# Optimization experiments

Measured on AMD Instinct MI355X. Metric: run time of the kernel, lower is better.

## Reference

```python
import jax, jax.numpy as jnp
import numpy as np
from jax import lax

N, C, H, W = 6, 64, 128, 128
BN_EPS = 1e-5


def setup_inputs() -> dict:
    key = jax.random.key(0)
    ks = jax.random.split(key, 16)
    def p(i, shape, scale=0.05):
        return jax.random.normal(ks[i], shape, jnp.float32) * scale
    return {
        "raw_feat": jax.random.normal(ks[0], (N, C, H, W), jnp.float32),
        # PixelWeightedFusionSoftmax params (1x1 convs stored as [out,in] matrices)
        "pw_w1": p(1, (4, C)), "pw_b1": p(2, (4,)),
        "bn_gamma": 1.0 + p(3, (4,)), "bn_beta": p(4, (4,)),
        "bn_mean": jnp.zeros((4,), jnp.float32), "bn_var": jnp.ones((4,), jnp.float32),
        "pw_w2": p(5, (1, 4)), "pw_b2": p(6, (1,)),
        # ConvMod params: a = dwconv11x11(gelu(conv1x1_{2C->C}(q))); out = proj(a * v(v) * att_map)
        "cm_a1_w": p(7, (C, 2 * C)), "cm_a1_b": p(8, (C,)),
        "cm_dw_w": p(9, (C, 1, 11, 11)), "cm_dw_b": p(10, (C,)),
        "cm_v_w": p(11, (C, C)), "cm_v_b": p(12, (C,)),
        "cm_proj_w": p(13, (C, C)), "cm_proj_b": p(14, (C,)),
    }


def _conf_maps(x, pw_w1, pw_b1, bn_gamma, bn_beta, bn_mean, bn_var, pw_w2, pw_b2):
    # x: [N,C,H,W] -> per-agent confidence maps [N,1,H,W], min-max normalized per agent
    h = jnp.einsum('nchw,oc->nohw', x, pw_w1) + pw_b1[:, None, None]
    scale = (bn_gamma / jnp.sqrt(bn_var + BN_EPS))[:, None, None]
    h = (h - bn_mean[:, None, None]) * scale + bn_beta[:, None, None]  # BN eval mode
    h = jax.nn.relu(h)
    h = jax.nn.relu(jnp.einsum('nchw,oc->nohw', h, pw_w2) + pw_b2[:, None, None])
    mn = h.min(axis=(1, 2, 3), keepdims=True)
    mx = h.max(axis=(1, 2, 3), keepdims=True)
    return (h - mn) / (mx - mn)


def reference(raw_feat, pw_w1, pw_b1, bn_gamma, bn_beta, bn_mean, bn_var, pw_w2, pw_b2,
              cm_a1_w, cm_a1_b, cm_dw_w, cm_dw_b, cm_v_w, cm_v_b, cm_proj_w, cm_proj_b):
    conf = _conf_maps(raw_feat, pw_w1, pw_b1, bn_gamma, bn_beta, bn_mean, bn_var, pw_w2, pw_b2)  # [N,1,H,W]
    # att_map[i,k] = (1 - conf_i) * conf_k
    att_map = (1.0 - conf)[:, None] * conf[None, :]  # [N,N,1,H,W]
    # q[i,k] = concat(raw[i], raw[k]) along channels -> [N,N,2C,H,W]
    q = jnp.concatenate([jnp.broadcast_to(raw_feat[:, None], (N, N, C, H, W)),
                         jnp.broadcast_to(raw_feat[None, :], (N, N, C, H, W))], axis=2)
    a = jax.nn.gelu(jnp.einsum('ikchw,oc->ikohw', q, cm_a1_w) + cm_a1_b[:, None, None],
                    approximate=False)
    a = lax.conv_general_dilated(a.reshape(N * N, C, H, W), cm_dw_w,
                                 window_strides=(1, 1), padding='SAME',
                                 feature_group_count=C,
                                 dimension_numbers=('NCHW', 'OIHW', 'NCHW'))
    a = a.reshape(N, N, C, H, W) + cm_dw_b[:, None, None]
    vproj = jnp.einsum('nchw,oc->nohw', raw_feat, cm_v_w) + cm_v_b[:, None, None]  # [N,C,H,W]
    x = a * vproj[None] * att_map  # [N,N,C,H,W]
    out = jnp.einsum('ikchw,oc->ikohw', x, cm_proj_w) + cm_proj_b[:, None, None]
    updated = raw_feat + out.sum(axis=1)  # ego i accumulates over all senders k
    return updated.reshape(N * C, H, W)   # matches torch.cat(local_com_mat_update, dim=0)
```

## Files before the change

### kernel.cpp

```cpp
#include <hip/hip_runtime.h>
#include <math.h>

#define NAG 6
#define CC  64
#define HH  128
#define WW  128
#define HWT 16384
#define HWP 8192
#define BN_EPS 1e-5f
#define WFRAG_PJ_OFF (24 * 64 * 8)

typedef unsigned int u32;
typedef __fp16 f16x2v __attribute__((ext_vector_type(2)));
typedef __fp16 f16x8  __attribute__((ext_vector_type(8)));
typedef float  f32x4  __attribute__((ext_vector_type(4)));

__device__ __forceinline__ float gelu_fast(float x) {
    float s = x * x;
    float m = fmaf(s, -0.10294535f, -2.30226045f);
    float e = __builtin_amdgcn_exp2f(x * m);
    return x * __builtin_amdgcn_rcpf(1.0f + e);
}

__global__ void k_init(u32* __restrict__ mm) {
    int t = threadIdx.x;
    if (t < NAG) mm[t] = 0x7F800000u;
    else if (t < 2 * NAG) mm[t] = 0u;
}

__global__ __launch_bounds__(256) void k_wprep(
    const float* __restrict__ a1w, const float* __restrict__ vw,
    const float* __restrict__ pjw, __fp16* __restrict__ wfrag)
{
    int t = blockIdx.x * 256 + threadIdx.x;
    if (t >= 32 * 64) return;
    int lane = t & 63;
    int slot = t >> 6;
    bool pj = slot >= 24;
    int s = pj ? slot - 24 : slot;
    int ot = s >> 1, kf = s & 1;
    int o  = (pj ? ot : (ot & 3)) * 16 + (lane & 15);
    int ch = kf * 32 + (lane >> 4) * 8;
    const float* src;
    if (pj)          src = pjw + o * CC + ch;
    else if (ot < 4) src = a1w + o * 2 * CC + ch;
    else if (ot < 8) src = a1w + o * 2 * CC + CC + ch;
    else             src = vw  + o * CC + ch;
    __fp16* dst = wfrag + ((size_t)slot * 64 + lane) * 8;
    #pragma unroll
    for (int j = 0; j < 8; ++j) dst[j] = (__fp16)src[j];
}

__global__ __launch_bounds__(256) void k_conf(
    const float* __restrict__ raw,
    const float* __restrict__ w1, const float* __restrict__ b1,
    const float* __restrict__ gamma, const float* __restrict__ beta,
    const float* __restrict__ mean, const float* __restrict__ var,
    const float* __restrict__ w2, const float* __restrict__ b2,
    float* __restrict__ conf, u32* __restrict__ mm)
{
    const int n = blockIdx.y;
    const int p = blockIdx.x * 256 + threadIdx.x;
    const float* x = raw + (size_t)(n * CC) * HWT + p;

    float a[4] = {0.f, 0.f, 0.f, 0.f};
    #pragma unroll 8
    for (int c = 0; c < CC; ++c) {
        float v = x[c * HWT];
        a[0] = fmaf(w1[0 * CC + c], v, a[0]);
        a[1] = fmaf(w1[1 * CC + c], v, a[1]);
        a[2] = fmaf(w1[2 * CC + c], v, a[2]);
        a[3] = fmaf(w1[3 * CC + c], v, a[3]);
    }
    float h2 = b2[0];
    #pragma unroll
    for (int o = 0; o < 4; ++o) {
        float sc = gamma[o] * rsqrtf(var[o] + BN_EPS);
        float hb = (a[o] + b1[o] - mean[o]) * sc + beta[o];
        hb = fmaxf(hb, 0.f);
        h2 = fmaf(w2[o], hb, h2);
    }
    h2 = fmaxf(h2, 0.f);
    conf[n * HWT + p] = h2;

    float mn = h2, mx = h2;
    #pragma unroll
    for (int off = 32; off > 0; off >>= 1) {
        mn = fminf(mn, __shfl_xor(mn, off, 64));
        mx = fmaxf(mx, __shfl_xor(mx, off, 64));
    }
    __shared__ float smn[4], smx[4];
    int wid = threadIdx.x >> 6, lane = threadIdx.x & 63;
    if (lane == 0) { smn[wid] = mn; smx[wid] = mx; }
    __syncthreads();
    if (threadIdx.x == 0) {
        mn = fminf(fminf(smn[0], smn[1]), fminf(smn[2], smn[3]));
        mx = fmaxf(fmaxf(smx[0], smx[1]), fmaxf(smx[2], smx[3]));
        atomicMin(&mm[n], __float_as_uint(mn));
        atomicMax(&mm[n + NAG], __float_as_uint(mx));
    }
}

__global__ __launch_bounds__(256) void k_pqv(
    const float* __restrict__ raw, const __fp16* __restrict__ wfrag,
    const float* __restrict__ vb, const float* __restrict__ conf,
    const u32* __restrict__ mm,
    u32* __restrict__ Ph, u32* __restrict__ Qh, u32* __restrict__ Wh)
{
    const int n   = blockIdx.y;
    const int px0 = blockIdx.x * 128;
    const int t = threadIdx.x, lane = t & 63, wv = t >> 6;
    const int lm = lane & 15, kg = lane >> 4;
    const int pxw = px0 + wv * 32;
    const int pxl = pxw + lm;
    const int pxs = pxw + kg * 4;

    const float* rawn = raw + (size_t)n * CC * HWT;

    f16x8 afr[2][2];
    #pragma unroll
    for (int mt = 0; mt < 2; ++mt) {
        #pragma unroll
        for (int kf = 0; kf < 2; ++kf) {
            const float* base = rawn + (size_t)(kf * 32 + kg * 8) * HWT + pxl + mt * 16;
            f16x8 a;
            #pragma unroll
            for (int p = 0; p < 4; ++p) {
                f16x2v h = __builtin_amdgcn_cvt_pkrtz(base[(2 * p) * HWT],
                                                      base[(2 * p + 1) * HWT]);
                a[2 * p] = h.x; a[2 * p + 1] = h.y;
            }
            afr[mt][kf] = a;
        }
    }

    const float mn = __uint_as_float(mm[n]);
    const float mx = __uint_as_float(mm[n + NAG]);
    const float inv = 1.f / (mx - mn);
    f32x4 cn[2];
    #pragma unroll
    for (int mt = 0; mt < 2; ++mt) {
        f32x4 cv = *(const f32x4*)(conf + n * HWT + pxs + mt * 16);
        cn[mt] = (cv - mn) * inv;
    }

    #pragma unroll
    for (int ot = 0; ot < 12; ++ot) {
        f16x8 b0 = *(const f16x8*)(wfrag + ((size_t)(ot * 2 + 0) * 64 + lane) * 8);
        f16x8 b1 = *(const f16x8*)(wfrag + ((size_t)(ot * 2 + 1) * 64 + lane) * 8);
        const int o = (ot & 3) * 16 + lm;
        #pragma unroll
        for (int mt = 0; mt < 2; ++mt) {
            f32x4 acc = (f32x4){0.f, 0.f, 0.f, 0.f};
            acc = __builtin_amdgcn_mfma_f32_16x16x32_f16(afr[mt][0], b0, acc, 0, 0, 0);
            acc = __builtin_amdgcn_mfma_f32_16x16x32_f16(afr[mt][1], b1, acc, 0, 0, 0);
            const int pxb = pxs + mt * 16;
            f32x4 r;
            u32* plane;
            if (ot < 8) {
                r = acc;
                plane = (ot < 4 ? Ph : Qh) + (size_t)(n * CC + o) * HWP + (pxb >> 1);
            } else {
                r = (acc + vb[o]) * cn[mt];
                plane = Wh + (size_t)(n * CC + o) * HWP + (pxb >> 1);
            }
            f16x2v h0 = __builtin_amdgcn_cvt_pkrtz(r[0], r[1]);
            f16x2v h1 = __builtin_amdgcn_cvt_pkrtz(r[2], r[3]);
            *(uint2*)plane = make_uint2(__builtin_bit_cast(u32, h0),
                                        __builtin_bit_cast(u32, h1));
        }
    }
}

#define GPITCH 88
#define GROWS  74
#define GDW    (GROWS * GPITCH / 2)
#define NU2    13

__global__ __launch_bounds__(256, 3) void k_main(
    const u32* __restrict__ Ph, const u32* __restrict__ Qh,
    const u32* __restrict__ Wh, const float* __restrict__ conf,
    const u32* __restrict__ mm,
    const float* __restrict__ a1b, const float* __restrict__ dww,
    const float* __restrict__ dwb, u32* __restrict__ Sh)
{
    const int tile = blockIdx.x;
    const int c    = blockIdx.y;
    const int i    = blockIdx.z;
    const int y0 = (tile >> 1) * 64;
    const int x0 = (tile & 1) * 64;
    const int t    = threadIdx.x;
    const int lane = t & 63;
    const int ty   = t >> 6;
    const int lm   = lane & 15;
    const int kg   = lane >> 4;
    const int kg8  = kg * 8;

    __shared__ __align__(16) u32 GT32[2 * GDW];

    const float bdw = dwb[c];
    const float ba1 = a1b[c];

    const float* wc = dww + c * 121;
    f16x8 afrag[11];
    #pragma unroll
    for (int dy = 0; dy < 11; ++dy) {
        f16x8 a;
        #pragma unroll
        for (int j = 0; j < 8; ++j) {
            int d = kg8 + j - lm - 3;
            int dcl = min(max(d, 0), 10);
            float wv = wc[dy * 11 + dcl];
            a[j] = (__fp16)((d == dcl) ? wv : 0.f);
        }
        afrag[dy] = a;
    }

    f16x2v bias2; bias2.x = (__fp16)ba1; bias2.y = (__fp16)ba1;

    int offs[NU2];
    u32 preg[NU2];
    const u32* Pc = Ph + (size_t)(i * CC + c) * HWP;
    #pragma unroll
    for (int u = 0; u < NU2; ++u) {
        int d = t + u * 256;
        int row = d / (GPITCH / 2);
        int cp  = d - row * (GPITCH / 2);
        int gy = y0 + row - 5;
        int gx = x0 + 2 * cp - 8;
        bool inb = (d < GDW) && (gy >= 0) && (gy < HH) && (gx >= 0) && (gx < WW);
        offs[u] = inb ? (gy * (WW / 2) + (gx >> 1)) : -1;
        u32 p = 0u;
        if (inb) {
            f16x2v ph = __builtin_bit_cast(f16x2v, Pc[offs[u]]) + bias2;
            p = __builtin_bit_cast(u32, ph);
        }
        preg[u] = p;
    }

    const int oy  = y0 + ty * 16 + lm;
    const int obx = x0 + kg * 4;
    const int obase = oy * WW + obx;
    const int rowb = (ty * 16 + lm) * GPITCH + kg8;

    f32x4 sacc[4];
    #pragma unroll
    for (int tx = 0; tx < 4; ++tx) sacc[tx] = (f32x4){0.f, 0.f, 0.f, 0.f};

    u32 qreg[NU2];
    {
        const u32* Qc = Qh + (size_t)(0 * CC + c) * HWP;
        #pragma unroll
        for (int u = 0; u < NU2; ++u)
            qreg[u] = (offs[u] >= 0) ? Qc[offs[u]] : 0u;
    }
    #pragma unroll
    for (int u = 0; u < NU2; ++u) {
        int d = t + u * 256;
        if (u < NU2 - 1 || d < GDW) {
            f16x2v s = __builtin_bit_cast(f16x2v, preg[u]) +
                       __builtin_bit_cast(f16x2v, qreg[u]);
            float g0 = gelu_fast((float)s.x);
            float g1 = gelu_fast((float)s.y);
            GT32[d] = __builtin_bit_cast(u32, __builtin_amdgcn_cvt_pkrtz(g0, g1));
        }
    }
    {
        const u32* Qc = Qh + (size_t)(1 * CC + c) * HWP;
        #pragma unroll
        for (int u = 0; u < NU2; ++u)
            qreg[u] = (offs[u] >= 0) ? Qc[offs[u]] : 0u;
    }
    __syncthreads();

    #pragma unroll 1
    for (int k = 0; k < NAG; ++k) {
        const u32* Wc = Wh + (size_t)(k * CC + c) * HWP + (obase >> 1);
        uint2 wv[4];
        #pragma unroll
        for (int tx = 0; tx < 4; ++tx)
            wv[tx] = *(const uint2*)(Wc + 8 * tx);

        const __fp16* GTh = (const __fp16*)(GT32 + (k & 1) * GDW);
        #pragma unroll
        for (int tx = 0; tx < 4; ++tx) {
            f32x4 acc = (f32x4){0.f, 0.f, 0.f, 0.f};
            #pragma unroll
            for (int dy = 0; dy < 11; ++dy) {
                f16x8 b = *(const f16x8*)(GTh + rowb + dy * GPITCH + 16 * tx);
                acc = __builtin_amdgcn_mfma_f32_16x16x32_f16(afrag[dy], b, acc, 0, 0, 0);
            }
            f16x2v w0 = __builtin_bit_cast(f16x2v, wv[tx].x);
            f16x2v w1 = __builtin_bit_cast(f16x2v, wv[tx].y);
            f32x4 wf = (f32x4){(float)w0.x, (float)w0.y, (float)w1.x, (float)w1.y};
            sacc[tx] += (acc + bdw) * wf;
        }

        if (k + 1 < NAG) {
            u32* GW = GT32 + ((k + 1) & 1) * GDW;
            #pragma unroll
            for (int u = 0; u < NU2; ++u) {
                int d = t + u * 256;
                if (u < NU2 - 1 || d < GDW) {
                    f16x2v s = __builtin_bit_cast(f16x2v, preg[u]) +
                               __builtin_bit_cast(f16x2v, qreg[u]);
                    float g0 = gelu_fast((float)s.x);
                    float g1 = gelu_fast((float)s.y);
                    GW[d] = __builtin_bit_cast(u32, __builtin_amdgcn_cvt_pkrtz(g0, g1));
                }
            }
            if (k + 2 < NAG) {
                const u32* Qc = Qh + (size_t)((k + 2) * CC + c) * HWP;
                #pragma unroll
                for (int u = 0; u < NU2; ++u)
                    qreg[u] = (offs[u] >= 0) ? Qc[offs[u]] : 0u;
            }
            __syncthreads();
        }
    }

    const float mn = __uint_as_float(mm[i]);
    const float mx = __uint_as_float(mm[i + NAG]);
    const float inv = 1.f / (mx - mn);
    const float* cfi = conf + i * HWT + obase;
    u32* Sc = Sh + (size_t)(i * CC + c) * HWP + (obase >> 1);
    #pragma unroll
    for (int tx = 0; tx < 4; ++tx) {
        f32x4 cv = *(const f32x4*)(cfi + 16 * tx);
        f32x4 r = sacc[tx] * (1.f - (cv - mn) * inv);
        f16x2v h0 = __builtin_amdgcn_cvt_pkrtz(r[0], r[1]);
        f16x2v h1 = __builtin_amdgcn_cvt_pkrtz(r[2], r[3]);
        *(uint2*)(Sc + 8 * tx) = make_uint2(__builtin_bit_cast(u32, h0),
                                            __builtin_bit_cast(u32, h1));
    }
}

__global__ __launch_bounds__(256) void k_out(
    const u32* __restrict__ Sh, const float* __restrict__ raw,
    const __fp16* __restrict__ wfrag, const float* __restrict__ pb,
    float* __restrict__ out)
{
    const int n   = blockIdx.y;
    const int px0 = blockIdx.x * 128;
    const int t = threadIdx.x, lane = t & 63, wv = t >> 6;
    const int lm = lane & 15, kg = lane >> 4;
    const int pxw = px0 + wv * 32;
    const int pxl = pxw + lm;
    const int pxs = pxw + kg * 4;

    const u32* Sn = Sh + (size_t)n * CC * HWP;
    const u32 sh = (pxl & 1) * 16;

    f16x8 afr[2][2];
    #pragma unroll
    for (int mt = 0; mt < 2; ++mt) {
        #pragma unroll
        for (int kf = 0; kf < 2; ++kf) {
            const u32* base = Sn + (size_t)(kf * 32 + kg * 8) * HWP + ((pxl + mt * 16) >> 1);
            f16x8 a;
            #pragma unroll
            for (int j = 0; j < 8; ++j) {
                unsigned short v = (unsigned short)(base[(size_t)j * HWP] >> sh);
                a[j] = __builtin_bit_cast(__fp16, v);
            }
            afr[mt][kf] = a;
        }
    }

    #pragma unroll
    for (int ot = 0; ot < 4; ++ot) {
        f16x8 b0 = *(const f16x8*)(wfrag + WFRAG_PJ_OFF +
                                   ((size_t)(ot * 2 + 0) * 64 + lane) * 8);
        f16x8 b1 = *(const f16x8*)(wfrag + WFRAG_PJ_OFF +
                                   ((size_t)(ot * 2 + 1) * 64 + lane) * 8);
        const int o = ot * 16 + lm;
        const float bias = (float)NAG * pb[o];
        #pragma unroll
        for (int mt = 0; mt < 2; ++mt) {
            f32x4 acc = (f32x4){0.f, 0.f, 0.f, 0.f};
            acc = __builtin_amdgcn_mfma_f32_16x16x32_f16(afr[mt][0], b0, acc, 0, 0, 0);
            acc = __builtin_amdgcn_mfma_f32_16x16x32_f16(afr[mt][1], b1, acc, 0, 0, 0);
            const int pxb = pxs + mt * 16;
            f32x4 r = *(const f32x4*)(raw + (size_t)(n * CC + o) * HWT + pxb);
            f32x4 ov = r + acc + bias;
            *(f32x4*)(out + (size_t)(n * CC + o) * HWT + pxb) = ov;
        }
    }
}

extern "C" void kernel_launch(void* const* d_in, const int* in_sizes, int n_in,
                              void* d_out, int out_size, void* d_ws, size_t ws_size,
                              hipStream_t stream)
{
    (void)in_sizes; (void)n_in; (void)out_size; (void)ws_size;

    const float* raw   = (const float*)d_in[0];
    const float* pw_w1 = (const float*)d_in[1];
    const float* pw_b1 = (const float*)d_in[2];
    const float* bng   = (const float*)d_in[3];
    const float* bnb   = (const float*)d_in[4];
    const float* bnm   = (const float*)d_in[5];
    const float* bnv   = (const float*)d_in[6];
    const float* pw_w2 = (const float*)d_in[7];
    const float* pw_b2 = (const float*)d_in[8];
    const float* a1w   = (const float*)d_in[9];
    const float* a1b   = (const float*)d_in[10];
    const float* dww   = (const float*)d_in[11];
    const float* dwb   = (const float*)d_in[12];
    const float* vw    = (const float*)d_in[13];
    const float* vb    = (const float*)d_in[14];
    const float* pjw   = (const float*)d_in[15];
    const float* pjb   = (const float*)d_in[16];

    float* ws   = (float*)d_ws;
    float* conf = ws;
    u32*   mm   = (u32*)(ws + NAG * HWT);
    u32*   Ph   = (u32*)(ws + NAG * HWT + 16);
    u32*   Qh   = Ph + (size_t)NAG * CC * HWP;
    u32*   Wh   = Qh + (size_t)NAG * CC * HWP;
    u32*   Sh   = Wh + (size_t)NAG * CC * HWP;
    __fp16* wfrag = (__fp16*)(Sh + (size_t)NAG * CC * HWP);
    float* out  = (float*)d_out;

    k_init<<<dim3(1), dim3(64), 0, stream>>>(mm);
    k_wprep<<<dim3(8), dim3(256), 0, stream>>>(a1w, vw, pjw, wfrag);
    k_conf<<<dim3(HWT / 256, NAG), dim3(256), 0, stream>>>(raw, pw_w1, pw_b1, bng, bnb,
                                                           bnm, bnv, pw_w2, pw_b2, conf, mm);
    k_pqv<<<dim3(HWT / 128, NAG), dim3(256), 0, stream>>>(raw, wfrag, vb, conf, mm,
                                                          Ph, Qh, Wh);
    k_main<<<dim3(4, CC, NAG), dim3(256), 0, stream>>>(Ph, Qh, Wh, conf, mm, a1b, dww, dwb, Sh);
    k_out<<<dim3(HWT / 128, NAG), dim3(256), 0, stream>>>(Sh, raw, wfrag, pjb, out);
}
```

Measured before the change: 111.7 us.

## Use packed half2 GELU, raise wave priority around MFMA loop, merge init kernels

Replaces the scalar fp32 GELU approximation with a packed half2 version, so two values are computed per instruction with no fp32 conversions. It also wraps the MFMA depthwise-conv loop in s_setprio to favour matrix work during scheduling. The init and weight-prep kernels are merged into one launch to save launch overhead. Computing GELU in fp16, including the exp2 of x*m, loses precision and can overflow for large-magnitude inputs.

```diff
diff --git a/kernel.cpp b/kernel.cpp
--- a/kernel.cpp
+++ b/kernel.cpp
@@ -1,4 +1,5 @@
 #include <hip/hip_runtime.h>
+#include <hip/hip_fp16.h>
 #include <math.h>
 
 #define NAG 6
@@ -15,24 +16,24 @@
 typedef __fp16 f16x8  __attribute__((ext_vector_type(8)));
 typedef float  f32x4  __attribute__((ext_vector_type(4)));
 
-__device__ __forceinline__ float gelu_fast(float x) {
-    float s = x * x;
-    float m = fmaf(s, -0.10294535f, -2.30226045f);
-    float e = __builtin_amdgcn_exp2f(x * m);
-    return x * __builtin_amdgcn_rcpf(1.0f + e);
-}
-
-__global__ void k_init(u32* __restrict__ mm) {
-    int t = threadIdx.x;
+__device__ __forceinline__ u32 gelu_pk(u32 xu) {
+    __half2 x = __builtin_bit_cast(__half2, xu);
+    __half2 s = __hmul2(x, x);
+    __half2 m = __hfma2(s, __float2half2_rn(-0.10294535f),
+                        __float2half2_rn(-2.30226045f));
+    __half2 e = h2exp2(__hmul2(x, m));
+    __half2 r = h2rcp(__hadd2(e, __float2half2_rn(1.0f)));
+    return __builtin_bit_cast(u32, __hmul2(x, r));
+}
+
+__global__ __launch_bounds__(256) void k_setup(
+    const float* __restrict__ a1w, const float* __restrict__ vw,
+    const float* __restrict__ pjw, __fp16* __restrict__ wfrag,
+    u32* __restrict__ mm)
+{
+    int t = blockIdx.x * 256 + threadIdx.x;
     if (t < NAG) mm[t] = 0x7F800000u;
-    else if (t < 2 * NAG) mm[t] = 0u;
-}
-
-__global__ __launch_bounds__(256) void k_wprep(
-    const float* __restrict__ a1w, const float* __restrict__ vw,
-    const float* __restrict__ pjw, __fp16* __restrict__ wfrag)
-{
-    int t = blockIdx.x * 256 + threadIdx.x;
+    else if (t < 2 * NAG && t >= NAG) mm[t] = 0u;
     if (t >= 32 * 64) return;
     int lane = t & 63;
     int slot = t >> 6;
@@ -260,9 +261,7 @@
         if (u < NU2 - 1 || d < GDW) {
             f16x2v s = __builtin_bit_cast(f16x2v, preg[u]) +
                        __builtin_bit_cast(f16x2v, qreg[u]);
-            float g0 = gelu_fast((float)s.x);
-            float g1 = gelu_fast((float)s.y);
-            GT32[d] = __builtin_bit_cast(u32, __builtin_amdgcn_cvt_pkrtz(g0, g1));
+            GT32[d] = gelu_pk(__builtin_bit_cast(u32, s));
         }
     }
     {
@@ -282,6 +281,7 @@
             wv[tx] = *(const uint2*)(Wc + 8 * tx);
 
         const __fp16* GTh = (const __fp16*)(GT32 + (k & 1) * GDW);
+        __builtin_amdgcn_s_setprio(1);
         #pragma unroll
         for (int tx = 0; tx < 4; ++tx) {
             f32x4 acc = (f32x4){0.f, 0.f, 0.f, 0.f};
@@ -295,6 +295,7 @@
             f32x4 wf = (f32x4){(float)w0.x, (float)w0.y, (float)w1.x, (float)w1.y};
             sacc[tx] += (acc + bdw) * wf;
         }
+        __builtin_amdgcn_s_setprio(0);
 
         if (k + 1 < NAG) {
             u32* GW = GT32 + ((k + 1) & 1) * GDW;
@@ -304,9 +305,7 @@
                 if (u < NU2 - 1 || d < GDW) {
                     f16x2v s = __builtin_bit_cast(f16x2v, preg[u]) +
                                __builtin_bit_cast(f16x2v, qreg[u]);
-                    float g0 = gelu_fast((float)s.x);
-                    float g1 = gelu_fast((float)s.y);
-                    GW[d] = __builtin_bit_cast(u32, __builtin_amdgcn_cvt_pkrtz(g0, g1));
+                    GW[d] = gelu_pk(__builtin_bit_cast(u32, s));
                 }
             }
             if (k + 2 < NAG) {
@@ -422,8 +421,7 @@
     __fp16* wfrag = (__fp16*)(Sh + (size_t)NAG * CC * HWP);
     float* out  = (float*)d_out;
 
-    k_init<<<dim3(1), dim3(64), 0, stream>>>(mm);
-    k_wprep<<<dim3(8), dim3(256), 0, stream>>>(a1w, vw, pjw, wfrag);
+    k_setup<<<dim3(8), dim3(256), 0, stream>>>(a1w, vw, pjw, wfrag, mm);
     k_conf<<<dim3(HWT / 256, NAG), dim3(256), 0, stream>>>(raw, pw_w1, pw_b1, bng, bnb,
                                                            bnm, bnv, pw_w2, pw_b2, conf, mm);
     k_pqv<<<dim3(HWT / 128, NAG), dim3(256), 0, stream>>>(raw, wfrag, vb, conf, mm,
```

Measured after the change: 108.1 us. -3.2%, faster.
